# Optimization experiments

Hardware: AMD Instinct MI355X
Metric: run time of the kernel (lower is better)

Reference implementation:

```python
import jax, jax.numpy as jnp
import numpy as np

B, L, T = 256, 256, 50  # batch, max_len, num_tags


def setup_inputs() -> dict:
    key = jax.random.key(0)
    k1, k2, k3 = jax.random.split(key, 3)
    feats = jax.random.normal(k1, (B, L, T), dtype=jnp.float32)
    trans_m = jax.random.normal(k2, (T, T), dtype=jnp.float32)
    tags = jax.random.randint(k3, (B, L), 0, T)
    mask = jnp.ones((B, L), dtype=jnp.int32)
    return {"feats": feats, "trans_m": trans_m, "tags": tags, "mask": mask}


def _normalizer(logits, trans_m, m):
    # logits: (L, B, T), m: (L, B) float mask
    alpha0 = logits[0]  # (B, T)

    def step(alpha, inp):
        emit, mt = inp  # (B, T), (B,)
        # (B, T_from, T_to) broadcast add, logsumexp over T_from
        tmp = alpha[:, :, None] + trans_m[None, :, :] + emit[:, None, :]
        new = jax.nn.logsumexp(tmp, axis=1)
        alpha = jnp.where(mt[:, None] > 0, new, alpha)
        return alpha, None

    alpha, _ = jax.lax.scan(step, alpha0, (logits[1:], m[1:]))
    return jax.nn.logsumexp(alpha, axis=1)  # (B,)


def _gold_score(logits, trans_m, tags_t, m):
    # logits: (L, B, T); tags_t: (L, B); m: (L, B)
    trans_sc = trans_m[tags_t[:-1], tags_t[1:]] * m[1:]  # (L-1, B)
    emit_sc = jnp.take_along_axis(logits, tags_t[:, :, None], axis=2)[..., 0] * m  # (L, B)
    return jnp.sum(trans_sc + emit_sc[:-1], axis=0) + emit_sc[-1]  # (B,)


def reference(feats, trans_m, tags, mask):
    # feats: (B, L, T) -> (L, B, T); include_start_end_trans=False
    logits = jnp.transpose(feats, (1, 0, 2))
    tags_t = tags.T
    m = mask.T.astype(feats.dtype)
    all_path = _normalizer(logits, trans_m, m)
    gold = _gold_score(logits, trans_m, tags_t, m)
    return all_path - gold  # (B,) loss per example
```

## Files before the change

kernel.cpp:

```cpp
#include <hip/hip_runtime.h>
#include <math.h>


#define TAGS 50
#define LEN 256
#define INV_LN2 1.4426950408889634f
#define LN2 0.6931471805599453f

typedef __attribute__((ext_vector_type(8))) short bf16x8;
typedef __attribute__((ext_vector_type(4))) float f32x4;

#if __has_builtin(__builtin_amdgcn_exp2f)
#define EXP2F(x) __builtin_amdgcn_exp2f(x)
#else
#define EXP2F(x) exp2f(x)
#endif
#if __has_builtin(__builtin_amdgcn_logf)
#define LOG2F(x) __builtin_amdgcn_logf(x)
#else
#define LOG2F(x) log2f(x)
#endif
#if __has_builtin(__builtin_amdgcn_rcpf)
#define RCPF(x) __builtin_amdgcn_rcpf(x)
#else
#define RCPF(x) (1.0f / (x))
#endif

__device__ __forceinline__ float readlane_f(float v, int srclane) {
  return __builtin_bit_cast(float,
      __builtin_amdgcn_readlane(__builtin_bit_cast(int, v), srclane));
}

__device__ __forceinline__ int bf16pair(float lo, float hi) {
  unsigned lb = (__builtin_bit_cast(unsigned, lo) + 0x8000u) >> 16;
  unsigned hb = (__builtin_bit_cast(unsigned, hi) + 0x8000u) & 0xFFFF0000u;
  return (int)(hb | lb);
}

__global__ __launch_bounds__(64) void crf_fwd_kernel(
    const float* __restrict__ feats,
    const float* __restrict__ trans,
    const int*   __restrict__ tags,
    const int*   __restrict__ mask,
    float*       __restrict__ out)
{
  const int b    = blockIdx.x;
  const int lane = threadIdx.x;
  const int toc  = lane < TAGS ? lane : (TAGS - 1);
  const int q    = lane >> 4;
  const int n    = lane & 15;

  __shared__ __align__(16) float feats_lds[LEN * TAGS];
  __shared__ int mask_lds[LEN];

  const float* fb = feats + (size_t)b * (LEN * TAGS);
  const int*   tb = tags + b * LEN;
  const int*   mb = mask + b * LEN;

  int tg_c[4], tg_p[4];
#pragma unroll
  for (int k = 0; k < 4; ++k) {
    const int p = lane + 64 * k;
    tg_c[k] = tb[p];
    tg_p[k] = (p >= 1) ? tb[p - 1] : 0;
  }

  {
    const float4* fv = (const float4*)fb;
    for (int i = lane; i < (LEN * TAGS) / 4; i += 64) {
      float4 v = fv[i];
      v.x *= INV_LN2; v.y *= INV_LN2; v.z *= INV_LN2; v.w *= INV_LN2;
      *(float4*)&feats_lds[i * 4] = v;
    }
    for (int i = lane; i < LEN; i += 64) mask_lds[i] = mb[i];
  }

  union U8 { int i[4]; bf16x8 v; };
  U8 Bfr[4][2];
#pragma unroll
  for (int t = 0; t < 4; ++t)
#pragma unroll
    for (int c = 0; c < 2; ++c)
#pragma unroll
      for (int r = 0; r < 4; ++r) {
        const int f0 = 32 * c + 8 * q + 2 * r;
        const int to = 16 * t + n;
        const float e0 = (f0 < TAGS && to < TAGS)
            ? EXP2F(trans[f0 * TAGS + to] * INV_LN2) : 0.0f;
        const float e1 = (f0 + 1 < TAGS && to < TAGS)
            ? EXP2F(trans[(f0 + 1) * TAGS + to] * INV_LN2) : 0.0f;
        Bfr[t][c].i[r] = bf16pair(e0, e1);
      }

  int addrA[2][4];
#pragma unroll
  for (int c = 0; c < 2; ++c)
#pragma unroll
    for (int r = 0; r < 4; ++r)
      addrA[c][r] = (32 * c + 8 * q + 2 * r) * 4;

  __syncthreads();

  const float padf = (lane < TAGS) ? 1.0f : 0.0f;
  const float e0 = feats_lds[toc];
  const float c0 = readlane_f(e0, 0);
  float v = EXP2F(e0 - c0) * padf;
  float S = c0;

  float ehat_nxt = EXP2F(feats_lds[TAGS + toc]) * padf;
  int   m_nxt = mask_lds[1];

  const f32x4 zero4 = {0.0f, 0.0f, 0.0f, 0.0f};

  for (int l = 1; l < LEN; ++l) {
    const float ehat = ehat_nxt;
    const int   m_cur = m_nxt;
    const int   ln = (l + 1 < LEN) ? (l + 1) : (LEN - 1);
    const float e_raw = feats_lds[ln * TAGS + toc];
    m_nxt = mask_lds[ln];

    const float partner = __shfl_xor(v, 1, 64);
    const float lo = (lane & 1) ? partner : v;
    const float hi = (lane & 1) ? v : partner;
    const int pk = bf16pair(lo, hi);

    U8 A0, A1;
#pragma unroll
    for (int r = 0; r < 4; ++r) {
      A0.i[r] = __builtin_amdgcn_ds_bpermute(addrA[0][r], pk);
      A1.i[r] = __builtin_amdgcn_ds_bpermute(addrA[1][r], pk);
    }

    f32x4 d0 = __builtin_amdgcn_mfma_f32_16x16x32_bf16(A0.v, Bfr[0][0].v, zero4, 0, 0, 0);
    f32x4 d1 = __builtin_amdgcn_mfma_f32_16x16x32_bf16(A0.v, Bfr[1][0].v, zero4, 0, 0, 0);
    f32x4 d2 = __builtin_amdgcn_mfma_f32_16x16x32_bf16(A0.v, Bfr[2][0].v, zero4, 0, 0, 0);
    f32x4 d3 = __builtin_amdgcn_mfma_f32_16x16x32_bf16(A0.v, Bfr[3][0].v, zero4, 0, 0, 0);
    d0 = __builtin_amdgcn_mfma_f32_16x16x32_bf16(A1.v, Bfr[0][1].v, d0, 0, 0, 0);
    d1 = __builtin_amdgcn_mfma_f32_16x16x32_bf16(A1.v, Bfr[1][1].v, d1, 0, 0, 0);
    d2 = __builtin_amdgcn_mfma_f32_16x16x32_bf16(A1.v, Bfr[2][1].v, d2, 0, 0, 0);
    d3 = __builtin_amdgcn_mfma_f32_16x16x32_bf16(A1.v, Bfr[3][1].v, d3, 0, 0, 0);

    const float p01 = (lane & 16) ? d1[0] : d0[0];
    const float p23 = (lane & 16) ? d3[0] : d2[0];
    const float d   = (lane & 32) ? p23 : p01;

    const float cand = d * ehat;
    const float vnew = (m_cur > 0) ? cand : v;
    const float cc = readlane_f(vnew, 0);
    const float rr = RCPF(cc);
    v = vnew * rr;
    S += LOG2F(cc);
    ehat_nxt = EXP2F(e_raw) * padf;
  }

  float sum = v;
#pragma unroll
  for (int off = 32; off; off >>= 1) sum += __shfl_xor(sum, off, 64);

  float gp = 0.0f;
#pragma unroll
  for (int k = 0; k < 4; ++k) {
    const int p = lane + 64 * k;
    if (mask_lds[p] > 0) {
      float vv = feats_lds[p * TAGS + tg_c[k]] * LN2;
      if (p >= 1) vv += trans[tg_p[k] * TAGS + tg_c[k]];
      gp += vv;
    }
  }
#pragma unroll
  for (int off = 32; off; off >>= 1) gp += __shfl_xor(gp, off, 64);

  if (lane == 0) {
    const float all_path = LN2 * (S + LOG2F(sum));
    out[b] = all_path - gp;
  }
}

extern "C" void kernel_launch(void* const* d_in, const int* in_sizes, int n_in,
                              void* d_out, int out_size, void* d_ws, size_t ws_size,
                              hipStream_t stream) {
  const float* feats = (const float*)d_in[0];
  const float* trans = (const float*)d_in[1];
  const int*   tags  = (const int*)d_in[2];
  const int*   mask  = (const int*)d_in[3];
  float* out = (float*)d_out;

  const int B = out_size;
  crf_fwd_kernel<<<B, 64, 0, stream>>>(feats, trans, tags, mask, out);
}
```

Measured before the change: 126.5 us.

## Keep alpha replicated in MFMA output layout to drop shuffle and select chain

Alpha is now held as four per-lane values that match the MFMA output tile layout: each lane owns tag columns n, n+16, n+32 and n+48. The packed bf16 A operand is built directly from these registers, with the trans B operand reordered to match. This removes the xor-shuffle and lane-select steps from the serial recurrence. The two K-halves now go into independent MFMA chains that are summed at the end, and the normaliser readlane/reciprocal is taken from the previous alpha so it runs off the critical path. In exchange, each lane does four times the elementwise exp and multiply work, and the final sum reduces over only 16 lanes.

```diff
diff --git a/kernel.cpp b/kernel.cpp
--- a/kernel.cpp
+++ b/kernel.cpp
@@ -46,7 +46,6 @@
 {
   const int b    = blockIdx.x;
   const int lane = threadIdx.x;
-  const int toc  = lane < TAGS ? lane : (TAGS - 1);
   const int q    = lane >> 4;
   const int n    = lane & 15;
 
@@ -68,13 +67,21 @@
   {
     const float4* fv = (const float4*)fb;
     for (int i = lane; i < (LEN * TAGS) / 4; i += 64) {
-      float4 v = fv[i];
-      v.x *= INV_LN2; v.y *= INV_LN2; v.z *= INV_LN2; v.w *= INV_LN2;
-      *(float4*)&feats_lds[i * 4] = v;
+      float4 v4 = fv[i];
+      v4.x *= INV_LN2; v4.y *= INV_LN2; v4.z *= INV_LN2; v4.w *= INV_LN2;
+      *(float4*)&feats_lds[i * 4] = v4;
     }
     for (int i = lane; i < LEN; i += 64) mask_lds[i] = mb[i];
   }
 
+  int tgl[4], tcl[4], vld[4];
+#pragma unroll
+  for (int t = 0; t < 4; ++t) {
+    tgl[t] = n + 16 * t;
+    vld[t] = tgl[t] < TAGS;
+    tcl[t] = vld[t] ? tgl[t] : (TAGS - 1);
+  }
+
   union U8 { int i[4]; bf16x8 v; };
   U8 Bfr[4][2];
 #pragma unroll
@@ -83,79 +90,84 @@
     for (int c = 0; c < 2; ++c)
 #pragma unroll
       for (int r = 0; r < 4; ++r) {
-        const int f0 = 32 * c + 8 * q + 2 * r;
-        const int to = 16 * t + n;
-        const float e0 = (f0 < TAGS && to < TAGS)
-            ? EXP2F(trans[f0 * TAGS + to] * INV_LN2) : 0.0f;
-        const float e1 = (f0 + 1 < TAGS && to < TAGS)
-            ? EXP2F(trans[(f0 + 1) * TAGS + to] * INV_LN2) : 0.0f;
+        const int col = 16 * t + n;
+        const int tag0 = 16 * c + 4 * q + r;
+        const int tag1 = tag0 + 32;
+        const float e0 = (tag0 < TAGS && col < TAGS)
+            ? EXP2F(trans[tag0 * TAGS + col] * INV_LN2) : 0.0f;
+        const float e1 = (tag1 < TAGS && col < TAGS)
+            ? EXP2F(trans[tag1 * TAGS + col] * INV_LN2) : 0.0f;
         Bfr[t][c].i[r] = bf16pair(e0, e1);
       }
 
-  int addrA[2][4];
-#pragma unroll
-  for (int c = 0; c < 2; ++c)
-#pragma unroll
-    for (int r = 0; r < 4; ++r)
-      addrA[c][r] = (32 * c + 8 * q + 2 * r) * 4;
+  int addr[4];
+#pragma unroll
+  for (int r = 0; r < 4; ++r) addr[r] = (4 * q + r) * 4;
 
   __syncthreads();
 
-  const float padf = (lane < TAGS) ? 1.0f : 0.0f;
-  const float e0 = feats_lds[toc];
-  const float c0 = readlane_f(e0, 0);
-  float v = EXP2F(e0 - c0) * padf;
+  const float c0 = feats_lds[0];
+  float v[4];
+#pragma unroll
+  for (int t = 0; t < 4; ++t)
+    v[t] = vld[t] ? EXP2F(feats_lds[tcl[t]] - c0) : 0.0f;
   float S = c0;
 
-  float ehat_nxt = EXP2F(feats_lds[TAGS + toc]) * padf;
-  int   m_nxt = mask_lds[1];
+  float eh[4];
+#pragma unroll
+  for (int t = 0; t < 4; ++t) eh[t] = EXP2F(feats_lds[TAGS + tcl[t]]);
+  int m_nxt = mask_lds[1];
 
   const f32x4 zero4 = {0.0f, 0.0f, 0.0f, 0.0f};
 
   for (int l = 1; l < LEN; ++l) {
-    const float ehat = ehat_nxt;
-    const int   m_cur = m_nxt;
-    const int   ln = (l + 1 < LEN) ? (l + 1) : (LEN - 1);
-    const float e_raw = feats_lds[ln * TAGS + toc];
-    m_nxt = mask_lds[ln];
-
-    const float partner = __shfl_xor(v, 1, 64);
-    const float lo = (lane & 1) ? partner : v;
-    const float hi = (lane & 1) ? v : partner;
-    const int pk = bf16pair(lo, hi);
+    const int m_cur = m_nxt;
+    const int ln = (l + 1 < LEN) ? (l + 1) : (LEN - 1);
+
+    const int P0 = bf16pair(v[0], v[2]);
+    const int P1 = bf16pair(v[1], v[3]);
+
+    const float cc = readlane_f(v[0], 0);
+    const float rr = RCPF(cc);
 
     U8 A0, A1;
 #pragma unroll
     for (int r = 0; r < 4; ++r) {
-      A0.i[r] = __builtin_amdgcn_ds_bpermute(addrA[0][r], pk);
-      A1.i[r] = __builtin_amdgcn_ds_bpermute(addrA[1][r], pk);
+      A0.i[r] = __builtin_amdgcn_ds_bpermute(addr[r], P0);
+      A1.i[r] = __builtin_amdgcn_ds_bpermute(addr[r], P1);
     }
 
     f32x4 d0 = __builtin_amdgcn_mfma_f32_16x16x32_bf16(A0.v, Bfr[0][0].v, zero4, 0, 0, 0);
     f32x4 d1 = __builtin_amdgcn_mfma_f32_16x16x32_bf16(A0.v, Bfr[1][0].v, zero4, 0, 0, 0);
     f32x4 d2 = __builtin_amdgcn_mfma_f32_16x16x32_bf16(A0.v, Bfr[2][0].v, zero4, 0, 0, 0);
     f32x4 d3 = __builtin_amdgcn_mfma_f32_16x16x32_bf16(A0.v, Bfr[3][0].v, zero4, 0, 0, 0);
-    d0 = __builtin_amdgcn_mfma_f32_16x16x32_bf16(A1.v, Bfr[0][1].v, d0, 0, 0, 0);
-    d1 = __builtin_amdgcn_mfma_f32_16x16x32_bf16(A1.v, Bfr[1][1].v, d1, 0, 0, 0);
-    d2 = __builtin_amdgcn_mfma_f32_16x16x32_bf16(A1.v, Bfr[2][1].v, d2, 0, 0, 0);
-    d3 = __builtin_amdgcn_mfma_f32_16x16x32_bf16(A1.v, Bfr[3][1].v, d3, 0, 0, 0);
-
-    const float p01 = (lane & 16) ? d1[0] : d0[0];
-    const float p23 = (lane & 16) ? d3[0] : d2[0];
-    const float d   = (lane & 32) ? p23 : p01;
-
-    const float cand = d * ehat;
-    const float vnew = (m_cur > 0) ? cand : v;
-    const float cc = readlane_f(vnew, 0);
-    const float rr = RCPF(cc);
-    v = vnew * rr;
+    f32x4 g0 = __builtin_amdgcn_mfma_f32_16x16x32_bf16(A1.v, Bfr[0][1].v, zero4, 0, 0, 0);
+    f32x4 g1 = __builtin_amdgcn_mfma_f32_16x16x32_bf16(A1.v, Bfr[1][1].v, zero4, 0, 0, 0);
+    f32x4 g2 = __builtin_amdgcn_mfma_f32_16x16x32_bf16(A1.v, Bfr[2][1].v, zero4, 0, 0, 0);
+    f32x4 g3 = __builtin_amdgcn_mfma_f32_16x16x32_bf16(A1.v, Bfr[3][1].v, zero4, 0, 0, 0);
+
+    float ehn[4];
+#pragma unroll
+    for (int t = 0; t < 4; ++t) ehn[t] = feats_lds[ln * TAGS + tcl[t]];
+    const int m_n2 = mask_lds[ln];
+
+    const float f0 = d0[0] + g0[0];
+    const float f1 = d1[0] + g1[0];
+    const float f2 = d2[0] + g2[0];
+    const float f3 = d3[0] + g3[0];
+    v[0] = ((m_cur > 0) ? f0 * eh[0] : v[0]) * rr;
+    v[1] = ((m_cur > 0) ? f1 * eh[1] : v[1]) * rr;
+    v[2] = ((m_cur > 0) ? f2 * eh[2] : v[2]) * rr;
+    v[3] = ((m_cur > 0) ? f3 * eh[3] : v[3]) * rr;
     S += LOG2F(cc);
-    ehat_nxt = EXP2F(e_raw) * padf;
-  }
-
-  float sum = v;
-#pragma unroll
-  for (int off = 32; off; off >>= 1) sum += __shfl_xor(sum, off, 64);
+#pragma unroll
+    for (int t = 0; t < 4; ++t) eh[t] = EXP2F(ehn[t]);
+    m_nxt = m_n2;
+  }
+
+  float vsum = (v[0] + v[1]) + (v[2] + v[3]);
+#pragma unroll
+  for (int off = 8; off; off >>= 1) vsum += __shfl_xor(vsum, off, 64);
 
   float gp = 0.0f;
 #pragma unroll
@@ -171,7 +183,7 @@
   for (int off = 32; off; off >>= 1) gp += __shfl_xor(gp, off, 64);
 
   if (lane == 0) {
-    const float all_path = LN2 * (S + LOG2F(sum));
+    const float all_path = LN2 * (S + LOG2F(vsum));
     out[b] = all_path - gp;
   }
 }
```

After: 131.8 us. +4.2%, slower.
